# Performance work log

Hardware: AMD Instinct MI355X
Metric: run time of the kernel (lower is better)

Reference implementation:

```python
import jax, jax.numpy as jnp
import numpy as np

N_EMBD = 768
N_HEAD = 12
HEAD_SIZE = N_EMBD // N_HEAD
LN_EPS = 1e-5


def setup_inputs() -> dict:
    key = jax.random.key(0)
    ks = jax.random.split(key, 12)
    s = 0.02
    B, T, C = 8, 1024, N_EMBD
    return {
        "x":  jax.random.normal(ks[0], (B, T, C), dtype=jnp.float32),
        # per-head q/k/v projections packed as [C, H*hs] (concat of head outputs)
        "Wq": jax.random.normal(ks[1], (C, C), dtype=jnp.float32) * s,
        "Wk": jax.random.normal(ks[2], (C, C), dtype=jnp.float32) * s,
        "Wv": jax.random.normal(ks[3], (C, C), dtype=jnp.float32) * s,
        "Wo": jax.random.normal(ks[4], (C, C), dtype=jnp.float32) * s,
        "bo": jnp.zeros((C,), dtype=jnp.float32),
        "W1": jax.random.normal(ks[5], (C, 4 * C), dtype=jnp.float32) * s,
        "b1": jnp.zeros((4 * C,), dtype=jnp.float32),
        "W2": jax.random.normal(ks[6], (4 * C, C), dtype=jnp.float32) * s,
        "b2": jnp.zeros((C,), dtype=jnp.float32),
        "g1": jnp.ones((C,), dtype=jnp.float32),
        "be1": jnp.zeros((C,), dtype=jnp.float32),
        "g2": jnp.ones((C,), dtype=jnp.float32),
        "be2": jnp.zeros((C,), dtype=jnp.float32),
    }


def _layernorm(x, g, b):
    mu = jnp.mean(x, axis=-1, keepdims=True)
    var = jnp.mean(jnp.square(x - mu), axis=-1, keepdims=True)
    return (x - mu) * jax.lax.rsqrt(var + LN_EPS) * g + b


def _block(x, Wq, Wk, Wv, Wo, bo, W1, b1, W2, b2, g1, be1, g2, be2):
    B, T, C = x.shape
    H, hs = N_HEAD, HEAD_SIZE
    h = _layernorm(x, g1, be1)
    q = (h @ Wq).reshape(B, T, H, hs)
    k = (h @ Wk).reshape(B, T, H, hs)
    v = (h @ Wv).reshape(B, T, H, hs)
    # NOTE: original code scales by n_embd**-0.5 (C from x.shape), not head_size**-0.5
    scores = jnp.einsum("bthd,bshd->bhts", q, k) * (C ** -0.5)
    causal = jnp.tril(jnp.ones((T, T), dtype=bool))  # [T,T]
    scores = jnp.where(causal, scores, -jnp.inf)
    attn = jax.nn.softmax(scores, axis=-1)  # [B,H,T,T]
    o = jnp.einsum("bhts,bshd->bthd", attn, v).reshape(B, T, C)
    x = x + o @ Wo + bo
    h2 = _layernorm(x, g2, be2)
    ff = jax.nn.gelu(h2 @ W1 + b1, approximate=False) @ W2 + b2
    return x + ff


def reference(x, Wq, Wk, Wv, Wo, bo, W1, b1, W2, b2, g1, be1, g2, be2):
    return _block(x, Wq, Wk, Wv, Wo, bo, W1, b1, W2, b2, g1, be1, g2, be2)
```

## Files before the change

kernel.cpp:

```cpp
#include <hip/hip_runtime.h>
#include <math.h>
#include <stdint.h>

typedef unsigned short u16;
typedef unsigned int u32;
typedef __attribute__((ext_vector_type(8))) __bf16 bf16x8;
typedef __attribute__((ext_vector_type(4))) float f32x4;

#define AS1 __attribute__((address_space(1)))
#define AS3 __attribute__((address_space(3)))

__device__ __forceinline__ void stage16(const void* g, void* l) {
    __builtin_amdgcn_global_load_lds((const AS1 void*)(uintptr_t)g,
                                     (AS3 void*)(uintptr_t)l, 16, 0, 0);
}

__device__ __forceinline__ u16 f2bf(float f) {
    u32 u = __float_as_uint(f);
    u += 0x7fffu + ((u >> 16) & 1u);
    return (u16)(u >> 16);
}

__global__ __launch_bounds__(256) void ln_kernel(const float* __restrict__ x,
                                                 const float* __restrict__ g,
                                                 const float* __restrict__ b,
                                                 u16* __restrict__ out) {
    int row = blockIdx.x;
    int tid = threadIdx.x;
    const float* xr = x + (size_t)row * 768;
    float x0 = xr[tid], x1 = xr[tid + 256], x2 = xr[tid + 512];

    __shared__ float red[256];
    red[tid] = x0 + x1 + x2;
    __syncthreads();
    for (int off = 128; off > 0; off >>= 1) {
        if (tid < off) red[tid] += red[tid + off];
        __syncthreads();
    }
    float mu = red[0] * (1.0f / 768.0f);
    __syncthreads();

    float d0 = x0 - mu, d1 = x1 - mu, d2 = x2 - mu;
    red[tid] = d0 * d0 + d1 * d1 + d2 * d2;
    __syncthreads();
    for (int off = 128; off > 0; off >>= 1) {
        if (tid < off) red[tid] += red[tid + off];
        __syncthreads();
    }
    float var = red[0] * (1.0f / 768.0f);
    float rs = rsqrtf(var + 1e-5f);

    u16* orow = out + (size_t)row * 768;
    orow[tid]       = f2bf(d0 * rs * g[tid]       + b[tid]);
    orow[tid + 256] = f2bf(d1 * rs * g[tid + 256] + b[tid + 256]);
    orow[tid + 512] = f2bf(d2 * rs * g[tid + 512] + b[tid + 512]);
}

__global__ __launch_bounds__(256) void transpose_bf16(const float* __restrict__ W,
                                                      u16* __restrict__ Wt,
                                                      int K, int N) {
    __shared__ float t[32][33];
    int tx = threadIdx.x, ty = threadIdx.y;
    int n0 = blockIdx.x * 32, k0 = blockIdx.y * 32;
#pragma unroll
    for (int j = 0; j < 32; j += 8)
        t[ty + j][tx] = W[(size_t)(k0 + ty + j) * N + n0 + tx];
    __syncthreads();
#pragma unroll
    for (int j = 0; j < 32; j += 8)
        Wt[(size_t)(n0 + ty + j) * K + k0 + tx] = f2bf(t[tx][ty + j]);
}

__global__ __launch_bounds__(256) void vt_kernel(const u16* __restrict__ qkv,
                                                 u16* __restrict__ Vt) {
    __shared__ u16 t[32][34];
    const int tx = threadIdx.x, ty = threadIdx.y;
    const int s0 = blockIdx.x * 32, d0 = blockIdx.y * 32, bh = blockIdx.z;
    const int b = bh / 12, h = bh % 12;
#pragma unroll
    for (int j = 0; j < 32; j += 8)
        t[ty + j][tx] = qkv[((size_t)(b * 1024) + s0 + ty + j) * 2304 + 1536 + h * 64 + d0 + tx];
    __syncthreads();
#pragma unroll
    for (int j = 0; j < 32; j += 8)
        Vt[((size_t)bh * 64 + d0 + ty + j) * 1024 + s0 + tx] = t[tx][ty + j];
}

__global__ __launch_bounds__(256) void mfma_gemm(
    const u16* __restrict__ A, const u16* __restrict__ Bt,
    const float* __restrict__ bias, const float* __restrict__ res,
    float* __restrict__ outF, u16* __restrict__ outB,
    int N, int K, int act) {
    __shared__ char lds[32768];
    const int tid = threadIdx.x, lane = tid & 63, wid = tid >> 6;
    const int l15 = lane & 15, lk = lane >> 4;
    const int wrow = (wid >> 1) * 64, wcol = (wid & 1) * 64;

    int wg = blockIdx.y * gridDim.x + blockIdx.x;
    const int nwg = gridDim.x * gridDim.y;
    wg = (wg & 7) * (nwg >> 3) + (wg >> 3);
    const int brow = (wg / gridDim.x) * 128;
    const int bcol = (wg % gridDim.x) * 128;

    const size_t K2 = (size_t)K * 2;
    const char* Abase = (const char*)A + (size_t)brow * K2;
    const char* Bbase = (const char*)Bt + (size_t)bcol * K2;

    int srow[2], scol[2];
#pragma unroll
    for (int j = 0; j < 2; ++j) {
        const int L = j * 4096 + tid * 16;
        srow[j] = L >> 6;
        scol[j] = (L & 63) ^ ((srow[j] & 3) << 4);
    }

    f32x4 acc[4][4] = {};
    const int nt = K >> 5;

#pragma unroll
    for (int j = 0; j < 2; ++j) {
        const size_t off = (size_t)srow[j] * K2 + scol[j];
        stage16(Abase + off, lds + j * 4096 + tid * 16);
        stage16(Bbase + off, lds + 8192 + j * 4096 + tid * 16);
    }
    __syncthreads();

    for (int t = 0; t < nt; ++t) {
        if (t + 1 < nt) {
            const char* An = Abase + (size_t)(t + 1) * 64;
            const char* Bn = Bbase + (size_t)(t + 1) * 64;
            char* dst = lds + ((t + 1) & 1) * 16384;
#pragma unroll
            for (int j = 0; j < 2; ++j) {
                const size_t off = (size_t)srow[j] * K2 + scol[j];
                stage16(An + off, dst + j * 4096 + tid * 16);
                stage16(Bn + off, dst + 8192 + j * 4096 + tid * 16);
            }
            asm volatile("s_waitcnt vmcnt(4)\n\ts_barrier" ::: "memory");
        } else {
            asm volatile("s_waitcnt vmcnt(0)\n\ts_barrier" ::: "memory");
        }
        __builtin_amdgcn_sched_barrier(0);

        const char* As = lds + (t & 1) * 16384;
        const char* Bs = As + 8192;
        bf16x8 af[4], bfv[4];
#pragma unroll
        for (int m = 0; m < 4; ++m) {
            const int row = wrow + m * 16 + l15;
            af[m] = *(const bf16x8*)(As + row * 64 + ((lk * 16) ^ ((row & 3) << 4)));
        }
#pragma unroll
        for (int n = 0; n < 4; ++n) {
            const int row = wcol + n * 16 + l15;
            bfv[n] = *(const bf16x8*)(Bs + row * 64 + ((lk * 16) ^ ((row & 3) << 4)));
        }
#pragma unroll
        for (int m = 0; m < 4; ++m)
#pragma unroll
            for (int n = 0; n < 4; ++n)
                acc[m][n] = __builtin_amdgcn_mfma_f32_16x16x32_bf16(af[m], bfv[n], acc[m][n], 0, 0, 0);

        asm volatile("s_barrier" ::: "memory");
    }

#pragma unroll
    for (int m = 0; m < 4; ++m)
#pragma unroll
        for (int n = 0; n < 4; ++n)
#pragma unroll
            for (int r = 0; r < 4; ++r) {
                int row = brow + wrow + m * 16 + lk * 4 + r;
                int col = bcol + wcol + n * 16 + l15;
                float v = acc[m][n][r];
                if (bias) v += bias[col];
                if (act) v = 0.5f * v * (1.0f + erff(v * 0.70710678118654752f));
                if (res) v += res[(size_t)row * N + col];
                if (outB) outB[(size_t)row * N + col] = f2bf(v);
                else outF[(size_t)row * N + col] = v;
            }
}

__global__ __launch_bounds__(256) void attn_mfma(const u16* __restrict__ qkv,
                                                 const u16* __restrict__ Vt,
                                                 u16* __restrict__ obf) {
    __shared__ char lds[40960];
    const int tid = threadIdx.x, lane = tid & 63, w = tid >> 6;
    const int g = lane >> 4, l15 = lane & 15;

    int wg = blockIdx.y * gridDim.x + blockIdx.x;
    const int nwg = gridDim.x * gridDim.y;
    wg = (wg & 7) * (nwg >> 3) + (wg >> 3);
    const int qb = 15 - (wg & 15);
    const int bh = wg >> 4;
    const int h = bh % 12, b = bh / 12;
    const int t0 = qb * 64;
    const float scale = 0.03608439182435161f;

    const size_t qrow = ((size_t)b * 1024 + t0 + 16 * w + l15) * 2304 + h * 64;
    const bf16x8 qf0 = *(const bf16x8*)(qkv + qrow + 8 * g);
    const bf16x8 qf1 = *(const bf16x8*)(qkv + qrow + 8 * g + 32);

    const int sub = ((lane & 7) * 16) ^ ((lane >> 3) << 4);
    const int r0 = 16 * w + (lane >> 3);
    const char* kSrc = (const char*)qkv + ((size_t)(b * 1024 + r0) * 2304 + 768 + h * 64) * 2 + sub;
    const char* vSrc = (const char*)Vt + ((size_t)(bh * 64 + r0) * 1024) * 2 + sub;
    const int dstOff = 2 * w * 1024 + lane * 16;

    stage16(kSrc,            lds + dstOff);
    stage16(kSrc + 8 * 4608, lds + dstOff + 1024);
    stage16(vSrc,            lds + 8192 + dstOff);
    stage16(vSrc + 8 * 2048, lds + 8192 + dstOff + 1024);
    kSrc += 64 * 4608; vSrc += 128;
    __syncthreads();

    const int swzA = (l15 & 7) << 4;
    float m_r[4] = {-1e30f, -1e30f, -1e30f, -1e30f};
    float l_r[4] = {0.f, 0.f, 0.f, 0.f};
    f32x4 oacc[4] = {};
    char* Pw = lds + 32768 + w * 2048;

    for (int c = 0; c <= qb; ++c) {
        if (c < qb) {
            char* dst = lds + ((c + 1) & 1) * 16384;
            stage16(kSrc,            dst + dstOff);
            stage16(kSrc + 8 * 4608, dst + dstOff + 1024);
            stage16(vSrc,            dst + 8192 + dstOff);
            stage16(vSrc + 8 * 2048, dst + 8192 + dstOff + 1024);
            kSrc += 64 * 4608; vSrc += 128;
            asm volatile("s_waitcnt vmcnt(4)\n\ts_barrier" ::: "memory");
        } else {
            asm volatile("s_waitcnt vmcnt(0)\n\ts_barrier" ::: "memory");
        }
        __builtin_amdgcn_sched_barrier(0);

        const char* bufK = lds + (c & 1) * 16384;
        const char* bufV = bufK + 8192;

        f32x4 sacc[4] = {};
#pragma unroll
        for (int st = 0; st < 4; ++st) {
            const char* krow = bufK + (l15 + 16 * st) * 128;
            const bf16x8 kf0 = *(const bf16x8*)(krow + ((16 * g) ^ swzA));
            const bf16x8 kf1 = *(const bf16x8*)(krow + ((16 * g + 64) ^ swzA));
            sacc[st] = __builtin_amdgcn_mfma_f32_16x16x32_bf16(qf0, kf0, sacc[st], 0, 0, 0);
            sacc[st] = __builtin_amdgcn_mfma_f32_16x16x32_bf16(qf1, kf1, sacc[st], 0, 0, 0);
        }

        const bool diag = (c == qb);
#pragma unroll
        for (int r = 0; r < 4; ++r) {
            float sv0 = sacc[0][r] * scale, sv1 = sacc[1][r] * scale;
            float sv2 = sacc[2][r] * scale, sv3 = sacc[3][r] * scale;
            if (diag) {
                const int trel = 16 * w + 4 * g + r;
                if (l15 +  0 > trel) sv0 = -1e30f;
                if (l15 + 16 > trel) sv1 = -1e30f;
                if (l15 + 32 > trel) sv2 = -1e30f;
                if (l15 + 48 > trel) sv3 = -1e30f;
            }
            float mx = fmaxf(fmaxf(sv0, sv1), fmaxf(sv2, sv3));
#pragma unroll
            for (int off = 1; off < 16; off <<= 1) mx = fmaxf(mx, __shfl_xor(mx, off));
            const float mnew = fmaxf(m_r[r], mx);
            const float corr = __expf(m_r[r] - mnew);
            const float p0 = __expf(sv0 - mnew), p1 = __expf(sv1 - mnew);
            const float p2 = __expf(sv2 - mnew), p3 = __expf(sv3 - mnew);
            float ps = p0 + p1 + p2 + p3;
#pragma unroll
            for (int off = 1; off < 16; off <<= 1) ps += __shfl_xor(ps, off);
            l_r[r] = l_r[r] * corr + ps;
            m_r[r] = mnew;
            oacc[0][r] *= corr; oacc[1][r] *= corr;
            oacc[2][r] *= corr; oacc[3][r] *= corr;
            const int q = 4 * g + r;
            char* pr = Pw + q * 128;
            const int sw = (q & 7) << 4;
            *(u16*)(pr + ((l15 * 2 +  0) ^ sw)) = f2bf(p0);
            *(u16*)(pr + ((l15 * 2 + 32) ^ sw)) = f2bf(p1);
            *(u16*)(pr + ((l15 * 2 + 64) ^ sw)) = f2bf(p2);
            *(u16*)(pr + ((l15 * 2 + 96) ^ sw)) = f2bf(p3);
        }

#pragma unroll
        for (int kc = 0; kc < 2; ++kc) {
            const bf16x8 pa = *(const bf16x8*)(Pw + l15 * 128 + ((16 * g + 64 * kc) ^ swzA));
#pragma unroll
            for (int dt = 0; dt < 4; ++dt) {
                const int d = l15 + 16 * dt;
                const bf16x8 vf = *(const bf16x8*)(bufV + d * 128 +
                                   ((16 * g + 64 * kc) ^ ((d & 7) << 4)));
                oacc[dt] = __builtin_amdgcn_mfma_f32_16x16x32_bf16(pa, vf, oacc[dt], 0, 0, 0);
            }
        }
        asm volatile("s_barrier" ::: "memory");
    }

    const size_t orow0 = ((size_t)b * 1024 + t0 + 16 * w) * 768 + h * 64;
#pragma unroll
    for (int r = 0; r < 4; ++r) {
        const float inv = 1.0f / l_r[r];
        const size_t orow = orow0 + (size_t)(4 * g + r) * 768;
#pragma unroll
        for (int dt = 0; dt < 4; ++dt)
            obf[orow + 16 * dt + l15] = f2bf(oacc[dt][r] * inv);
    }
}

extern "C" void kernel_launch(void* const* d_in, const int* in_sizes, int n_in,
                              void* d_out, int out_size, void* d_ws, size_t ws_size,
                              hipStream_t stream) {
    const float* x   = (const float*)d_in[0];
    const float* Wq  = (const float*)d_in[1];
    const float* Wk  = (const float*)d_in[2];
    const float* Wv  = (const float*)d_in[3];
    const float* Wo  = (const float*)d_in[4];
    const float* bo  = (const float*)d_in[5];
    const float* W1  = (const float*)d_in[6];
    const float* b1  = (const float*)d_in[7];
    const float* W2  = (const float*)d_in[8];
    const float* b2  = (const float*)d_in[9];
    const float* g1  = (const float*)d_in[10];
    const float* be1 = (const float*)d_in[11];
    const float* g2  = (const float*)d_in[12];
    const float* be2 = (const float*)d_in[13];
    float* out = (float*)d_out;

    char* ws = (char*)d_ws;
    u16* qkv_bf = (u16*)(ws);
    u16* ff1_bf = (u16*)(ws);
    float* x2   = (float*)(ws + 50331648);
    u16* h_bf   = (u16*)(ws + 75497472);
    u16* o_bf   = (u16*)(ws + 88080384);
    u16* Wqkvt  = (u16*)(ws + 100663296);
    u16* W1t    = (u16*)(ws + 104202240);
    u16* W2t    = (u16*)(ws + 108920832);
    u16* Wot    = (u16*)(ws + 113639424);
    u16* Vt     = (u16*)(ws + 114819072);

    dim3 tb(32, 8);
    transpose_bf16<<<dim3(24, 24), tb, 0, stream>>>(Wq, Wqkvt, 768, 768);
    transpose_bf16<<<dim3(24, 24), tb, 0, stream>>>(Wk, Wqkvt + 768 * 768, 768, 768);
    transpose_bf16<<<dim3(24, 24), tb, 0, stream>>>(Wv, Wqkvt + 2 * 768 * 768, 768, 768);
    transpose_bf16<<<dim3(24, 24), tb, 0, stream>>>(Wo, Wot, 768, 768);
    transpose_bf16<<<dim3(96, 24), tb, 0, stream>>>(W1, W1t, 768, 3072);
    transpose_bf16<<<dim3(24, 96), tb, 0, stream>>>(W2, W2t, 3072, 768);

    ln_kernel<<<8192, 256, 0, stream>>>(x, g1, be1, h_bf);
    mfma_gemm<<<dim3(18, 64), 256, 0, stream>>>(h_bf, Wqkvt, nullptr, nullptr, nullptr, qkv_bf, 2304, 768, 0);
    vt_kernel<<<dim3(32, 2, 96), tb, 0, stream>>>(qkv_bf, Vt);
    attn_mfma<<<dim3(16, 96), 256, 0, stream>>>(qkv_bf, Vt, o_bf);
    mfma_gemm<<<dim3(6, 64), 256, 0, stream>>>(o_bf, Wot, bo, x, x2, nullptr, 768, 768, 0);
    ln_kernel<<<8192, 256, 0, stream>>>(x2, g2, be2, h_bf);
    mfma_gemm<<<dim3(24, 64), 256, 0, stream>>>(h_bf, W1t, b1, nullptr, nullptr, ff1_bf, 3072, 768, 1);
    mfma_gemm<<<dim3(6, 64), 256, 0, stream>>>(ff1_bf, W2t, b2, x2, out, nullptr, 768, 3072, 0);
}
```

Before: 375.3 us.

## Triple-buffer GEMM LDS staging and change swizzle to reduce bank conflicts

Changes the GEMM mainloop from double to triple buffering in LDS. The tile for step t+2 is issued after the barrier, which removes the trailing barrier in each iteration. The LDS XOR swizzle now uses row bits 1-2 instead of bits 0-1, aiming to cut bank conflicts on the 16-byte fragment reads. It also raises wave priority around the MFMA block and sets launch bounds for 3 blocks per CU. In exchange, LDS use goes to 48KB per block, which may limit occupancy.

```diff
diff --git a/kernel.cpp b/kernel.cpp
--- a/kernel.cpp
+++ b/kernel.cpp
@@ -86,12 +86,12 @@
         Vt[((size_t)bh * 64 + d0 + ty + j) * 1024 + s0 + tx] = t[tx][ty + j];
 }
 
-__global__ __launch_bounds__(256) void mfma_gemm(
+__global__ __launch_bounds__(256, 3) void gemm_k32(
     const u16* __restrict__ A, const u16* __restrict__ Bt,
     const float* __restrict__ bias, const float* __restrict__ res,
     float* __restrict__ outF, u16* __restrict__ outB,
     int N, int K, int act) {
-    __shared__ char lds[32768];
+    __shared__ char lds[49152];
     const int tid = threadIdx.x, lane = tid & 63, wid = tid >> 6;
     const int l15 = lane & 15, lk = lane >> 4;
     const int wrow = (wid >> 1) * 64, wcol = (wid & 1) * 64;
@@ -111,57 +111,54 @@
     for (int j = 0; j < 2; ++j) {
         const int L = j * 4096 + tid * 16;
         srow[j] = L >> 6;
-        scol[j] = (L & 63) ^ ((srow[j] & 3) << 4);
-    }
+        scol[j] = (L & 63) ^ (((srow[j] >> 1) & 3) << 4);
+    }
+
+    const int nt = K >> 5;
+
+    auto stage_tile = [&](int t, char* dst) {
+#pragma unroll
+        for (int j = 0; j < 2; ++j) {
+            const size_t off = (size_t)srow[j] * K2 + (size_t)t * 64 + scol[j];
+            stage16(Abase + off, dst + j * 4096 + tid * 16);
+            stage16(Bbase + off, dst + 8192 + j * 4096 + tid * 16);
+        }
+    };
 
     f32x4 acc[4][4] = {};
-    const int nt = K >> 5;
-
-#pragma unroll
-    for (int j = 0; j < 2; ++j) {
-        const size_t off = (size_t)srow[j] * K2 + scol[j];
-        stage16(Abase + off, lds + j * 4096 + tid * 16);
-        stage16(Bbase + off, lds + 8192 + j * 4096 + tid * 16);
-    }
-    __syncthreads();
+
+    stage_tile(0, lds);
+    stage_tile(1, lds + 16384);
 
     for (int t = 0; t < nt; ++t) {
-        if (t + 1 < nt) {
-            const char* An = Abase + (size_t)(t + 1) * 64;
-            const char* Bn = Bbase + (size_t)(t + 1) * 64;
-            char* dst = lds + ((t + 1) & 1) * 16384;
-#pragma unroll
-            for (int j = 0; j < 2; ++j) {
-                const size_t off = (size_t)srow[j] * K2 + scol[j];
-                stage16(An + off, dst + j * 4096 + tid * 16);
-                stage16(Bn + off, dst + 8192 + j * 4096 + tid * 16);
-            }
-            asm volatile("s_waitcnt vmcnt(4)\n\ts_barrier" ::: "memory");
-        } else {
-            asm volatile("s_waitcnt vmcnt(0)\n\ts_barrier" ::: "memory");
-        }
+        if (t + 1 < nt) asm volatile("s_waitcnt vmcnt(4)\n\ts_barrier" ::: "memory");
+        else            asm volatile("s_waitcnt vmcnt(0)\n\ts_barrier" ::: "memory");
         __builtin_amdgcn_sched_barrier(0);
 
-        const char* As = lds + (t & 1) * 16384;
+        if (t + 2 < nt) stage_tile(t + 2, lds + ((t + 2) % 3) * 16384);
+
+        const char* As = lds + (t % 3) * 16384;
         const char* Bs = As + 8192;
         bf16x8 af[4], bfv[4];
 #pragma unroll
         for (int m = 0; m < 4; ++m) {
             const int row = wrow + m * 16 + l15;
-            af[m] = *(const bf16x8*)(As + row * 64 + ((lk * 16) ^ ((row & 3) << 4)));
+            af[m] = *(const bf16x8*)(As + row * 64 +
+                                     ((lk * 16) ^ (((row >> 1) & 3) << 4)));
         }
 #pragma unroll
         for (int n = 0; n < 4; ++n) {
             const int row = wcol + n * 16 + l15;
-            bfv[n] = *(const bf16x8*)(Bs + row * 64 + ((lk * 16) ^ ((row & 3) << 4)));
-        }
+            bfv[n] = *(const bf16x8*)(Bs + row * 64 +
+                                      ((lk * 16) ^ (((row >> 1) & 3) << 4)));
+        }
+        __builtin_amdgcn_s_setprio(1);
 #pragma unroll
         for (int m = 0; m < 4; ++m)
 #pragma unroll
             for (int n = 0; n < 4; ++n)
                 acc[m][n] = __builtin_amdgcn_mfma_f32_16x16x32_bf16(af[m], bfv[n], acc[m][n], 0, 0, 0);
-
-        asm volatile("s_barrier" ::: "memory");
+        __builtin_amdgcn_s_setprio(0);
     }
 
 #pragma unroll
@@ -347,11 +344,11 @@
     transpose_bf16<<<dim3(24, 96), tb, 0, stream>>>(W2, W2t, 3072, 768);
 
     ln_kernel<<<8192, 256, 0, stream>>>(x, g1, be1, h_bf);
-    mfma_gemm<<<dim3(18, 64), 256, 0, stream>>>(h_bf, Wqkvt, nullptr, nullptr, nullptr, qkv_bf, 2304, 768, 0);
+    gemm_k32<<<dim3(18, 64), 256, 0, stream>>>(h_bf, Wqkvt, nullptr, nullptr, nullptr, qkv_bf, 2304, 768, 0);
     vt_kernel<<<dim3(32, 2, 96), tb, 0, stream>>>(qkv_bf, Vt);
     attn_mfma<<<dim3(16, 96), 256, 0, stream>>>(qkv_bf, Vt, o_bf);
-    mfma_gemm<<<dim3(6, 64), 256, 0, stream>>>(o_bf, Wot, bo, x, x2, nullptr, 768, 768, 0);
+    gemm_k32<<<dim3(6, 64), 256, 0, stream>>>(o_bf, Wot, bo, x, x2, nullptr, 768, 768, 0);
     ln_kernel<<<8192, 256, 0, stream>>>(x2, g2, be2, h_bf);
-    mfma_gemm<<<dim3(24, 64), 256, 0, stream>>>(h_bf, W1t, b1, nullptr, nullptr, ff1_bf, 3072, 768, 1);
-    mfma_gemm<<<dim3(6, 64), 256, 0, stream>>>(ff1_bf, W2t, b2, x2, out, nullptr, 768, 3072, 0);
-}
+    gemm_k32<<<dim3(24, 64), 256, 0, stream>>>(h_bf, W1t, b1, nullptr, nullptr, ff1_bf, 3072, 768, 1);
+    gemm_k32<<<dim3(6, 64), 256, 0, stream>>>(ff1_bf, W2t, b2, x2, out, nullptr, 768, 3072, 0);
+}
```

New measurement: 373.9 us. Within noise of the previous version (-0.4%).
